# Kernel tuning notes

Hardware: AMD Instinct MI355X
Metric: run time of the kernel (lower is better)

The kernel has to match this reference:

```python
import jax, jax.numpy as jnp
import numpy as np

NUM_BANDS, B, K, D = 5, 512, 64, 200
H = 4            # num attention heads
HID = 512        # selector hidden width
S = 0.02         # weight init scale


def setup_inputs() -> dict:
    key = jax.random.key(0)
    ks = jax.random.split(key, 8)
    F_IN = NUM_BANDS * K * D  # 64000
    return {
        "bands": jax.random.normal(ks[0], (NUM_BANDS, B, K, D), jnp.float32),
        "w1": jax.random.normal(ks[1], (HID, F_IN), jnp.float32) * S,
        "b1": jnp.zeros((HID,), jnp.float32),
        "w2": jax.random.normal(ks[2], (NUM_BANDS, HID), jnp.float32) * S,
        "b2": jnp.zeros((NUM_BANDS,), jnp.float32),
        "in_proj_w": jax.random.normal(ks[3], (3 * D, D), jnp.float32) * S,
        "in_proj_b": jnp.zeros((3 * D,), jnp.float32),
        "out_w": jax.random.normal(ks[4], (D, D), jnp.float32) * S,
        "out_b": jnp.zeros((D,), jnp.float32),
    }


def reference(bands, w1, b1, w2, b2, in_proj_w, in_proj_b, out_w, out_b):
    nb, Bb, k, d = bands.shape
    hd = d // H
    scale = 1.0 / np.sqrt(hd)

    # concat(bands, dim=1): [B, nb*k, d] in band-major order
    x = jnp.transpose(bands, (1, 0, 2, 3))           # [B, nb, k, d]
    kv_in = x.reshape(Bb, nb * k, d)                 # [B, nb*k, d]

    # router MLP + softmax + argmax band select
    flat = kv_in.reshape(Bb, -1)                     # [B, nb*k*d]
    h = jax.nn.relu(flat @ w1.T + b1)                # [B, HID]
    band_weights = jax.nn.softmax(h @ w2.T + b2, axis=-1)
    sel = jnp.argmax(band_weights, axis=-1)          # [B] int

    # gather selected band per sample as the query
    Q = bands[sel, jnp.arange(Bb)]                   # [B, k, d]

    # multihead cross-attention (torch nn.MultiheadAttention math)
    wq, wk, wv = jnp.split(in_proj_w, 3, axis=0)
    bq, bk, bv = jnp.split(in_proj_b, 3, axis=0)
    q = (Q @ wq.T + bq).reshape(Bb, k, H, hd).transpose(0, 2, 1, 3)        # [B,H,k,hd]
    kk = (kv_in @ wk.T + bk).reshape(Bb, nb * k, H, hd).transpose(0, 2, 1, 3)
    v = (kv_in @ wv.T + bv).reshape(Bb, nb * k, H, hd).transpose(0, 2, 1, 3)

    attn = jax.nn.softmax(jnp.einsum('bhqe,bhke->bhqk', q, kk) * scale, axis=-1)
    o = jnp.einsum('bhqk,bhke->bhqe', attn, v)       # [B,H,k,hd]
    o = o.transpose(0, 2, 1, 3).reshape(Bb, k, d)
    return o @ out_w.T + out_b                        # [B, k, d]
```

## Files before the change

### kernel.cpp

```cpp
#include <hip/hip_runtime.h>
#include <hip/hip_bf16.h>

#define NBANDS 5
#define BATCH  512
#define KQN    64
#define DM     200
#define NHEAD  4
#define HD     50
#define HIDW   512
#define TKV    320
#define FIN    64000
#define KSPLIT 20
#define KCH    3200
#define RCH    50
#define NTT    13
#define KST    7
#define NTKV   25

typedef __bf16  bf16x8 __attribute__((ext_vector_type(8)));
typedef float   f32x4  __attribute__((ext_vector_type(4)));

static __device__ inline unsigned short f2bf(float f) {
    __hip_bfloat16 h = __float2bfloat16(f);
    return *reinterpret_cast<unsigned short*>(&h);
}
static __device__ inline float bf2f(unsigned short u) {
    union { unsigned int i; float f; } x;
    x.i = ((unsigned int)u) << 16;
    return x.f;
}
static __device__ inline bf16x8 bf8zero() {
    union { bf16x8 v; unsigned int u[4]; } z;
    z.u[0] = z.u[1] = z.u[2] = z.u[3] = 0u;
    return z.v;
}
static __device__ inline void split8(const float4& a, const float4& b,
                                     bf16x8& hi, bf16x8& lo) {
    union { bf16x8 v; unsigned short u[8]; } H, L;
    const float xs[8] = {a.x, a.y, a.z, a.w, b.x, b.y, b.z, b.w};
#pragma unroll
    for (int i = 0; i < 8; ++i) {
        H.u[i] = f2bf(xs[i]);
        L.u[i] = f2bf(xs[i] - bf2f(H.u[i]));
    }
    hi = H.v; lo = L.v;
}
static __device__ inline bf16x8 round8(const float4& a, const float4& b) {
    union { bf16x8 v; unsigned short u[8]; } H;
    const float xs[8] = {a.x, a.y, a.z, a.w, b.x, b.y, b.z, b.w};
#pragma unroll
    for (int i = 0; i < 8; ++i) H.u[i] = f2bf(xs[i]);
    return H.v;
}

__global__ __launch_bounds__(256) void k_router_mfma(
    const float* __restrict__ bands, const float* __restrict__ w1,
    float* __restrict__ part)
{
    __shared__ __align__(16) unsigned short Ah[64][72];
    __shared__ __align__(16) unsigned short Al[64][72];
    __shared__ __align__(16) unsigned short Bh[64][72];
    __shared__ __align__(16) unsigned short Bl[64][72];

    const int lin     = (blockIdx.z << 6) + (blockIdx.y << 3) + blockIdx.x;
    const int logical = (lin & 7) * 160 + (lin >> 3);
    const int z   = logical >> 6;
    const int rem = logical & 63;
    const int j0  = (rem & 7) << 6;
    const int b0  = (rem >> 3) << 6;

    const int t  = threadIdx.x;
    const int w  = t >> 6, lane = t & 63;
    const int lm = lane & 15, quad = lane >> 4;
    const int m0 = w * 16;

    const int row0 = t >> 4, c4 = (t & 15) * 4;

    f32x4 acc[4];
#pragma unroll
    for (int nt = 0; nt < 4; ++nt) acc[nt] = (f32x4){0.f, 0.f, 0.f, 0.f};

    const int kbase = z * KCH;
    for (int chunk = 0; chunk < RCH; ++chunk) {
        const int kc = kbase + chunk * 64;
        const int band = kc / 12800;
        const float* abase = bands + (size_t)band * 6540800 + kc + c4;
        const float* bbase = w1 + (size_t)j0 * FIN + kc + c4;
        float4 av[4], bv[4];
#pragma unroll
        for (int r = 0; r < 4; ++r)
            av[r] = *(const float4*)(abase + (size_t)(b0 + row0 + r * 16) * 12800);
#pragma unroll
        for (int r = 0; r < 4; ++r)
            bv[r] = *(const float4*)(bbase + (size_t)(row0 + r * 16) * FIN);
        __syncthreads();
#pragma unroll
        for (int r = 0; r < 4; ++r) {
            const int row = row0 + r * 16;
            ushort4 hh, ll;
            hh.x = f2bf(av[r].x); ll.x = f2bf(av[r].x - bf2f(hh.x));
            hh.y = f2bf(av[r].y); ll.y = f2bf(av[r].y - bf2f(hh.y));
            hh.z = f2bf(av[r].z); ll.z = f2bf(av[r].z - bf2f(hh.z));
            hh.w = f2bf(av[r].w); ll.w = f2bf(av[r].w - bf2f(hh.w));
            *(ushort4*)&Ah[row][c4] = hh;
            *(ushort4*)&Al[row][c4] = ll;
        }
#pragma unroll
        for (int r = 0; r < 4; ++r) {
            const int row = row0 + r * 16;
            ushort4 hh, ll;
            hh.x = f2bf(bv[r].x); ll.x = f2bf(bv[r].x - bf2f(hh.x));
            hh.y = f2bf(bv[r].y); ll.y = f2bf(bv[r].y - bf2f(hh.y));
            hh.z = f2bf(bv[r].z); ll.z = f2bf(bv[r].z - bf2f(hh.z));
            hh.w = f2bf(bv[r].w); ll.w = f2bf(bv[r].w - bf2f(hh.w));
            *(ushort4*)&Bh[row][c4] = hh;
            *(ushort4*)&Bl[row][c4] = ll;
        }
        __syncthreads();
#pragma unroll
        for (int ks = 0; ks < 2; ++ks) {
            const int ka = ks * 32 + quad * 8;
            const bf16x8 a_h = *(const bf16x8*)&Ah[m0 + lm][ka];
            const bf16x8 a_l = *(const bf16x8*)&Al[m0 + lm][ka];
#pragma unroll
            for (int nt = 0; nt < 4; ++nt) {
                const bf16x8 b_h = *(const bf16x8*)&Bh[nt * 16 + lm][ka];
                const bf16x8 b_l = *(const bf16x8*)&Bl[nt * 16 + lm][ka];
                acc[nt] = __builtin_amdgcn_mfma_f32_16x16x32_bf16(a_h, b_h, acc[nt], 0, 0, 0);
                acc[nt] = __builtin_amdgcn_mfma_f32_16x16x32_bf16(a_l, b_h, acc[nt], 0, 0, 0);
                acc[nt] = __builtin_amdgcn_mfma_f32_16x16x32_bf16(a_h, b_l, acc[nt], 0, 0, 0);
            }
        }
    }
    float* po = part + (size_t)z * (BATCH * HIDW);
#pragma unroll
    for (int nt = 0; nt < 4; ++nt) {
        const int jj = j0 + nt * 16 + lm;
#pragma unroll
        for (int reg = 0; reg < 4; ++reg) {
            const int bb = b0 + m0 + quad * 4 + reg;
            po[(size_t)bb * HIDW + jj] = acc[nt][reg];
        }
    }
}

__global__ __launch_bounds__(256) void k_reduce_relu(
    const float* __restrict__ part, const float* __restrict__ b1,
    float* __restrict__ h)
{
    const int tid = blockIdx.x * 256 + threadIdx.x;
    float s = b1[tid & (HIDW - 1)];
#pragma unroll
    for (int z = 0; z < KSPLIT; ++z) s += part[z * (BATCH * HIDW) + tid];
    h[tid] = fmaxf(s, 0.f);
}

__global__ __launch_bounds__(256) void k_wpack(
    const float* __restrict__ ipw, const float* __restrict__ outw,
    unsigned short* __restrict__ WqHp, unsigned short* __restrict__ WqLp,
    unsigned short* __restrict__ OwHp, unsigned short* __restrict__ OwLp)
{
    const int p = blockIdx.x;
    const int ks = p / NTT, nt = p - ks * NTT;
    const int t = threadIdx.x;
    const int lane = t >> 2, e0 = (t & 3) * 2;
    const int lm = lane & 15, quad = lane >> 4;
    const int row = nt * 16 + lm;
    const int k  = ks * 32 + quad * 8 + e0;
    const float* src = (blockIdx.y == 0) ? ipw : outw;
    unsigned short* dh = (blockIdx.y == 0) ? WqHp : OwHp;
    unsigned short* dl = (blockIdx.y == 0) ? WqLp : OwLp;
    float v0 = 0.f, v1 = 0.f;
    if (row < DM && k < DM) {
        v0 = src[(size_t)row * DM + k];
        v1 = src[(size_t)row * DM + k + 1];
    }
    const int off = (p << 9) + (lane << 3) + e0;
    const unsigned short h0 = f2bf(v0), h1 = f2bf(v1);
    dh[off]     = h0;
    dh[off + 1] = h1;
    dl[off]     = f2bf(v0 - bf2f(h0));
    dl[off + 1] = f2bf(v1 - bf2f(h1));
}

__global__ __launch_bounds__(256) void k_wpack_kv(
    const float* __restrict__ ipw, unsigned short* __restrict__ Wkv)
{
    const int p = blockIdx.x;
    const int ks = p / NTKV, nt = p - ks * NTKV;
    const int t = threadIdx.x;
    const int lane = t >> 2, e0 = (t & 3) * 2;
    const int lm = lane & 15, quad = lane >> 4;
    const int row = nt * 16 + lm;
    const int k  = ks * 32 + quad * 8 + e0;
    float v0 = 0.f, v1 = 0.f;
    if (k < DM) {
        v0 = ipw[(size_t)(DM + row) * DM + k];
        v1 = ipw[(size_t)(DM + row) * DM + k + 1];
    }
    const int off = (p << 9) + (lane << 3) + e0;
    Wkv[off]     = f2bf(v0);
    Wkv[off + 1] = f2bf(v1);
}

__global__ __launch_bounds__(256) void k_argmax(
    const float* __restrict__ h, const float* __restrict__ w2,
    const float* __restrict__ b2, int* __restrict__ sel)
{
    __shared__ float red[NBANDS][256];
    const int b = blockIdx.x, t = threadIdx.x;
    float acc[NBANDS] = {0.f, 0.f, 0.f, 0.f, 0.f};
    for (int j = t; j < HIDW; j += 256) {
        const float hv = h[b * HIDW + j];
#pragma unroll
        for (int n = 0; n < NBANDS; ++n)
            acc[n] = fmaf(hv, w2[n * HIDW + j], acc[n]);
    }
#pragma unroll
    for (int n = 0; n < NBANDS; ++n) red[n][t] = acc[n];
    __syncthreads();
    for (int s = 128; s > 0; s >>= 1) {
        if (t < s) {
#pragma unroll
            for (int n = 0; n < NBANDS; ++n) red[n][t] += red[n][t + s];
        }
        __syncthreads();
    }
    if (t == 0) {
        int best = 0;
        float bv = red[0][0] + b2[0];
        for (int n = 1; n < NBANDS; ++n) {
            const float v = red[n][0] + b2[n];
            if (v > bv) { bv = v; best = n; }
        }
        sel[b] = best;
    }
}

template<bool BF16OUT>
static __device__ inline void proj_core(
    const float* __restrict__ x0,
    const unsigned short* __restrict__ Ph,
    const unsigned short* __restrict__ Pl,
    const float* __restrict__ bias,
    void* __restrict__ outp)
{
    const int t = threadIdx.x;
    const int w = t >> 6, lane = t & 63;
    const int lm = lane & 15, quad = lane >> 4;
    const int m0 = w * 16;
    const float* xrow = x0 + (size_t)(m0 + lm) * DM;

    f32x4 acc[NTT];
#pragma unroll
    for (int nt = 0; nt < NTT; ++nt) acc[nt] = (f32x4){0.f, 0.f, 0.f, 0.f};

#pragma unroll
    for (int ks = 0; ks < KST; ++ks) {
        const int k0 = ks * 32 + quad * 8;
        bf16x8 a_h = bf8zero(), a_l = bf8zero();
        if (k0 + 8 <= DM) {
            const float4 xa = *(const float4*)(xrow + k0);
            const float4 xb = *(const float4*)(xrow + k0 + 4);
            split8(xa, xb, a_h, a_l);
        }
        const unsigned short* ph = Ph + ((ks * NTT) << 9) + (lane << 3);
        const unsigned short* pl = Pl + ((ks * NTT) << 9) + (lane << 3);
#pragma unroll
        for (int nt = 0; nt < NTT; ++nt) {
            const bf16x8 b_h = *(const bf16x8*)(ph + (nt << 9));
            const bf16x8 b_l = *(const bf16x8*)(pl + (nt << 9));
            acc[nt] = __builtin_amdgcn_mfma_f32_16x16x32_bf16(a_h, b_h, acc[nt], 0, 0, 0);
            acc[nt] = __builtin_amdgcn_mfma_f32_16x16x32_bf16(a_l, b_h, acc[nt], 0, 0, 0);
            acc[nt] = __builtin_amdgcn_mfma_f32_16x16x32_bf16(a_h, b_l, acc[nt], 0, 0, 0);
        }
    }
#pragma unroll
    for (int nt = 0; nt < NTT; ++nt) {
        const int col = nt * 16 + lm;
        if (col < DM) {
            const float bs = bias[col];
#pragma unroll
            for (int reg = 0; reg < 4; ++reg) {
                const int row = m0 + quad * 4 + reg;
                const float v = acc[nt][reg] + bs;
                if (BF16OUT)
                    ((unsigned short*)outp)[(size_t)row * DM + col] = f2bf(v);
                else
                    ((float*)outp)[(size_t)row * DM + col] = v;
            }
        }
    }
}

__global__ __launch_bounds__(256) void k_qproj_mfma(
    const float* __restrict__ bands, const int* __restrict__ sel,
    const unsigned short* __restrict__ WqHp, const unsigned short* __restrict__ WqLp,
    const float* __restrict__ ipb, unsigned short* __restrict__ qb)
{
    const int b = blockIdx.x;
    const int band = sel[b];
    const float* x0 = bands + (size_t)((band * BATCH + b) * KQN) * DM;
    proj_core<true>(x0, WqHp, WqLp, ipb, qb + (size_t)(b * KQN) * DM);
}

__global__ __launch_bounds__(256) void k_outproj_mfma(
    const float* __restrict__ obuf, const unsigned short* __restrict__ OwHp,
    const unsigned short* __restrict__ OwLp, const float* __restrict__ outb,
    float* __restrict__ out)
{
    const int b = blockIdx.x;
    proj_core<false>(obuf + (size_t)(b * KQN) * DM, OwHp, OwLp, outb,
                     out + (size_t)(b * KQN) * DM);
}

__global__ __launch_bounds__(256) void k_kvproj_lds(
    const float* __restrict__ bands, const unsigned short* __restrict__ Wkv,
    const float* __restrict__ ipb, __hip_bfloat16* __restrict__ Kp,
    __hip_bfloat16* __restrict__ Vp)
{
    __shared__ __align__(16) unsigned short Bs[2][NTKV * 512];
    const int t = threadIdx.x;
    const int w = t >> 6, lane = t & 63;
    const int lm = lane & 15, quad = lane >> 4;
    const int m0 = w * 16;
    const int M0 = blockIdx.x * 64;

    const int gg = M0 + m0 + lm;
    const int bb = gg / TKV, tk = gg - bb * TKV;
    const int band = tk >> 6, kk = tk & 63;
    const float* xrow = bands + (size_t)((band * BATCH + bb) * KQN + kk) * DM;

    float4 ar[2 * KST];
#pragma unroll
    for (int ks = 0; ks < KST; ++ks) {
        const int k0 = ks * 32 + quad * 8;
        if (k0 + 8 <= DM) {
            ar[2 * ks]     = *(const float4*)(xrow + k0);
            ar[2 * ks + 1] = *(const float4*)(xrow + k0 + 4);
        }
    }
    bf16x8 a[KST];
#pragma unroll
    for (int ks = 0; ks < KST; ++ks) {
        const int k0 = ks * 32 + quad * 8;
        a[ks] = (k0 + 8 <= DM) ? round8(ar[2 * ks], ar[2 * ks + 1]) : bf8zero();
    }

    auto stage = [&](int ks, int buf) {
        const unsigned short* src = Wkv + ((ks * NTKV) << 9);
#pragma unroll
        for (int pass = 0; pass < 6; ++pass) {
            const int i = pass * 256 + t;
            __builtin_amdgcn_global_load_lds(
                (const __attribute__((address_space(1))) unsigned int*)(src + (size_t)i * 8),
                (__attribute__((address_space(3))) unsigned int*)&Bs[buf][(pass * 256 + w * 64) * 8],
                16, 0, 0);
        }
        if (t < 64) {
            __builtin_amdgcn_global_load_lds(
                (const __attribute__((address_space(1))) unsigned int*)(src + (size_t)(1536 + lane) * 8),
                (__attribute__((address_space(3))) unsigned int*)&Bs[buf][1536 * 8],
                16, 0, 0);
        }
    };

    f32x4 acc[NTKV];
#pragma unroll
    for (int nt = 0; nt < NTKV; ++nt) acc[nt] = (f32x4){0.f, 0.f, 0.f, 0.f};

    stage(0, 0);
    __syncthreads();
#pragma unroll
    for (int ks = 0; ks < KST; ++ks) {
        if (ks + 1 < KST) stage(ks + 1, (ks + 1) & 1);
        const unsigned short* bs = &Bs[ks & 1][lane * 8];
#pragma unroll
        for (int nt = 0; nt < NTKV; ++nt) {
            const bf16x8 b8 = *(const bf16x8*)(bs + (nt << 9));
            acc[nt] = __builtin_amdgcn_mfma_f32_16x16x32_bf16(a[ks], b8, acc[nt], 0, 0, 0);
        }
        __syncthreads();
    }

#pragma unroll
    for (int nt = 0; nt < NTKV; ++nt) {
        const int col = nt * 16 + lm;
        const float bias = ipb[DM + col];
#pragma unroll
        for (int reg = 0; reg < 4; ++reg) {
            const int grow = M0 + m0 + quad * 4 + reg;
            const float v = acc[nt][reg] + bias;
            if (col < DM) Kp[(size_t)grow * DM + col] = __float2bfloat16(v);
            else          Vp[(size_t)grow * DM + (col - DM)] = __float2bfloat16(v);
        }
    }
}

__global__ __launch_bounds__(256) void k_attn(
    const unsigned short* __restrict__ qb, const __hip_bfloat16* __restrict__ Kp,
    const __hip_bfloat16* __restrict__ Vp, float* __restrict__ obuf)
{
    __shared__ __align__(16) unsigned short Qs[64][72];
    __shared__ __align__(16) unsigned short KP[320][72];
    __shared__ __align__(16) unsigned short Vt[64][328];
    __shared__ __align__(16) unsigned short Ps[64][328];
    const int b = blockIdx.x, hh = blockIdx.y;
    const int t = threadIdx.x;

    const unsigned short* qbase = qb + (size_t)(b * KQN) * DM + hh * HD;
    for (int idx = t; idx < 64 * 64; idx += 256) {
        const int r = idx >> 6, e = idx & 63;
        Qs[r][e] = (e < HD) ? qbase[(size_t)r * DM + e] : 0;
    }
    const unsigned short* kbase = (const unsigned short*)Kp + (size_t)b * TKV * DM + hh * HD;
    for (int idx = t; idx < 320 * 25; idx += 256) {
        const int key = idx / 25, g = idx - key * 25;
        *(unsigned int*)&KP[key][g * 2] =
            *(const unsigned int*)(kbase + (size_t)key * DM + g * 2);
    }
    for (int idx = t; idx < 320 * 7; idx += 256) {
        const int key = idx / 7, g = idx - key * 7;
        *(unsigned int*)&KP[key][50 + g * 2] = 0;
    }
    const unsigned short* vbase = (const unsigned short*)Vp + (size_t)b * TKV * DM + hh * HD;
    for (int idx = t; idx < 320 * 25; idx += 256) {
        const int key = idx / 25, g = idx - key * 25;
        const unsigned int v = *(const unsigned int*)(vbase + (size_t)key * DM + g * 2);
        Vt[g * 2][key]     = (unsigned short)(v & 0xffffu);
        Vt[g * 2 + 1][key] = (unsigned short)(v >> 16);
    }
    __syncthreads();

    const int w = t >> 6, lane = t & 63;
    const int lm = lane & 15, quad = lane >> 4;
    const int m0 = w * 16;

    f32x4 s[20];
#pragma unroll
    for (int nt = 0; nt < 20; ++nt) s[nt] = (f32x4){0.f, 0.f, 0.f, 0.f};
#pragma unroll
    for (int ks = 0; ks < 2; ++ks) {
        const int ka = ks * 32 + quad * 8;
        const bf16x8 a = *(const bf16x8*)&Qs[m0 + lm][ka];
#pragma unroll
        for (int nt = 0; nt < 20; ++nt) {
            const bf16x8 bb8 = *(const bf16x8*)&KP[nt * 16 + lm][ka];
            s[nt] = __builtin_amdgcn_mfma_f32_16x16x32_bf16(a, bb8, s[nt], 0, 0, 0);
        }
    }

    const float scale = 0.14142135623730951f;
    float inv[4];
#pragma unroll
    for (int reg = 0; reg < 4; ++reg) {
        float mx = -1e30f;
#pragma unroll
        for (int nt = 0; nt < 20; ++nt) {
            const float sv = s[nt][reg] * scale;
            s[nt][reg] = sv;
            mx = fmaxf(mx, sv);
        }
#pragma unroll
        for (int off = 1; off < 16; off <<= 1)
            mx = fmaxf(mx, __shfl_xor(mx, off, 64));
        float lsum = 0.f;
#pragma unroll
        for (int nt = 0; nt < 20; ++nt) {
            const float p = __expf(s[nt][reg] - mx);
            s[nt][reg] = p;
            lsum += p;
        }
#pragma unroll
        for (int off = 1; off < 16; off <<= 1)
            lsum += __shfl_xor(lsum, off, 64);
        inv[reg] = 1.f / lsum;
    }
#pragma unroll
    for (int reg = 0; reg < 4; ++reg) {
        const int row = m0 + quad * 4 + reg;
#pragma unroll
        for (int nt = 0; nt < 20; ++nt)
            Ps[row][nt * 16 + lm] = f2bf(s[nt][reg]);
    }
    __syncthreads();

    f32x4 o[4];
#pragma unroll
    for (int nt = 0; nt < 4; ++nt) o[nt] = (f32x4){0.f, 0.f, 0.f, 0.f};
#pragma unroll
    for (int ks = 0; ks < 10; ++ks) {
        const int ka = ks * 32 + quad * 8;
        const bf16x8 a = *(const bf16x8*)&Ps[m0 + lm][ka];
#pragma unroll
        for (int nt = 0; nt < 4; ++nt) {
            const bf16x8 bb8 = *(const bf16x8*)&Vt[nt * 16 + lm][ka];
            o[nt] = __builtin_amdgcn_mfma_f32_16x16x32_bf16(a, bb8, o[nt], 0, 0, 0);
        }
    }
    float* op = obuf + (size_t)(b * KQN) * DM + hh * HD;
#pragma unroll
    for (int nt = 0; nt < 4; ++nt) {
        const int e = nt * 16 + lm;
        if (e < HD) {
#pragma unroll
            for (int reg = 0; reg < 4; ++reg) {
                const int row = m0 + quad * 4 + reg;
                op[(size_t)row * DM + e] = o[nt][reg] * inv[reg];
            }
        }
    }
}

extern "C" void kernel_launch(void* const* d_in, const int* in_sizes, int n_in,
                              void* d_out, int out_size, void* d_ws, size_t ws_size,
                              hipStream_t stream)
{
    const float* bands = (const float*)d_in[0];
    const float* w1    = (const float*)d_in[1];
    const float* b1    = (const float*)d_in[2];
    const float* w2    = (const float*)d_in[3];
    const float* b2    = (const float*)d_in[4];
    const float* ipw   = (const float*)d_in[5];
    const float* ipb   = (const float*)d_in[6];
    const float* outw  = (const float*)d_in[7];
    const float* outb  = (const float*)d_in[8];
    float* out = (float*)d_out;

    if (ws_size < (size_t)192940032) return;

    char* ws = (char*)d_ws;
    int*   sel  = (int*)  (ws + 0);
    float* part = (float*)(ws + 4096);
    float* h    = (float*)(ws + 20975616);
    unsigned short* qb = (unsigned short*)(ws + 4096);
    unsigned short* Wkv  = (unsigned short*)(ws + 26218496);
    unsigned short* WqHp = (unsigned short*)(ws + 26404096);
    unsigned short* WqLp = (unsigned short*)(ws + 26497280);
    unsigned short* OwHp = (unsigned short*)(ws + 26590464);
    unsigned short* OwLp = (unsigned short*)(ws + 26683648);
    __hip_bfloat16* Kp = (__hip_bfloat16*)(ws + 26776832);
    __hip_bfloat16* Vp = (__hip_bfloat16*)(ws + 92312832);
    float* obuf = (float*)(ws + 157848832);

    k_wpack_kv<<<KST * NTKV, 256, 0, stream>>>(ipw, Wkv);
    k_wpack<<<dim3(KST * NTT, 2), 256, 0, stream>>>(ipw, outw, WqHp, WqLp, OwHp, OwLp);

    k_router_mfma<<<dim3(8, 8, KSPLIT), 256, 0, stream>>>(bands, w1, part);
    k_reduce_relu<<<(BATCH * HIDW) / 256, 256, 0, stream>>>(part, b1, h);
    k_argmax<<<BATCH, 256, 0, stream>>>(h, w2, b2, sel);
    k_qproj_mfma<<<BATCH, 256, 0, stream>>>(bands, sel, WqHp, WqLp, ipb, qb);
    k_kvproj_lds<<<2560, 256, 0, stream>>>(bands, Wkv, ipb, Kp, Vp);
    k_attn<<<dim3(BATCH, NHEAD), 256, 0, stream>>>(qb, Kp, Vp, obuf);
    k_outproj_mfma<<<BATCH, 256, 0, stream>>>(obuf, OwHp, OwLp, outb, out);
}
```

Before: 782.8 us.

## Pre-split w1 into MFMA-packed bf16 hi/lo tiles and drop LDS from router GEMM

Adds a kernel that converts w1 once per call into hi/lo bf16 halves stored in MFMA fragment order. The router GEMM then reads B fragments straight from global memory and splits A in registers, with no LDS staging or barriers. It also widens the tile to 64x128, doubles the K-split to 40, and sets launch bounds to 3 blocks per SM. The intent is to avoid converting w1 repeatedly across batch tiles and to remove sync overhead, at the cost of an extra 128MB of packed-weight traffic, more partial sums to reduce, and global loads that are no longer shared through LDS.

```diff
diff --git a/kernel.cpp b/kernel.cpp
--- a/kernel.cpp
+++ b/kernel.cpp
@@ -10,9 +10,10 @@
 #define HIDW   512
 #define TKV    320
 #define FIN    64000
-#define KSPLIT 20
-#define KCH    3200
-#define RCH    50
+#define BSTRIDE 6553600
+#define KSPLIT 40
+#define KCH    1600
+#define RCH    25
 #define NTT    13
 #define KST    7
 #define NTKV   25
@@ -53,88 +54,101 @@
     return H.v;
 }
 
-__global__ __launch_bounds__(256) void k_router_mfma(
-    const float* __restrict__ bands, const float* __restrict__ w1,
-    float* __restrict__ part)
-{
-    __shared__ __align__(16) unsigned short Ah[64][72];
-    __shared__ __align__(16) unsigned short Al[64][72];
-    __shared__ __align__(16) unsigned short Bh[64][72];
-    __shared__ __align__(16) unsigned short Bl[64][72];
-
-    const int lin     = (blockIdx.z << 6) + (blockIdx.y << 3) + blockIdx.x;
+__global__ __launch_bounds__(256) void k_splitw1(
+    const float* __restrict__ w1, unsigned short* __restrict__ BHp,
+    unsigned short* __restrict__ BLp)
+{
+    __shared__ __align__(16) unsigned short Hs[128][72];
+    __shared__ __align__(16) unsigned short Ls[128][72];
+    const int kc = blockIdx.x;
+    const int jt = blockIdx.y;
+    const int t  = threadIdx.x;
+    const int rl0 = t >> 4, cl4 = (t & 15) * 4;
+#pragma unroll
+    for (int i = 0; i < 8; ++i) {
+        const int row = rl0 + i * 16;
+        const float4 v = *(const float4*)(w1
+            + (size_t)(jt * 128 + row) * FIN + kc * 64 + cl4);
+        ushort4 hh, ll;
+        hh.x = f2bf(v.x); ll.x = f2bf(v.x - bf2f(hh.x));
+        hh.y = f2bf(v.y); ll.y = f2bf(v.y - bf2f(hh.y));
+        hh.z = f2bf(v.z); ll.z = f2bf(v.z - bf2f(hh.z));
+        hh.w = f2bf(v.w); ll.w = f2bf(v.w - bf2f(hh.w));
+        *(ushort4*)&Hs[row][cl4] = hh;
+        *(ushort4*)&Ls[row][cl4] = ll;
+    }
+    __syncthreads();
+    const size_t tbase = ((size_t)(jt * 1000 + kc)) << 13;
+#pragma unroll
+    for (int i = 0; i < 4; ++i) {
+        const int slot = i * 256 + t;
+        const int ksnt = slot >> 6, lane = slot & 63;
+        const int ks = ksnt >> 3, nt = ksnt & 7;
+        const int row = nt * 16 + (lane & 15);
+        const int col = ks * 32 + (lane >> 4) * 8;
+        *(uint4*)(BHp + tbase + (size_t)slot * 8) = *(const uint4*)&Hs[row][col];
+        *(uint4*)(BLp + tbase + (size_t)slot * 8) = *(const uint4*)&Ls[row][col];
+    }
+}
+
+__global__ __launch_bounds__(256, 3) void k_router_mfma(
+    const float* __restrict__ bands, const unsigned short* __restrict__ BHp,
+    const unsigned short* __restrict__ BLp, float* __restrict__ part)
+{
+    const int lin = (blockIdx.z << 5) | (blockIdx.y << 2) | blockIdx.x;
     const int logical = (lin & 7) * 160 + (lin >> 3);
-    const int z   = logical >> 6;
-    const int rem = logical & 63;
-    const int j0  = (rem & 7) << 6;
-    const int b0  = (rem >> 3) << 6;
-
-    const int t  = threadIdx.x;
-    const int w  = t >> 6, lane = t & 63;
+    const int z   = logical >> 5;
+    const int rem = logical & 31;
+    const int bt  = rem >> 2, jt = rem & 3;
+    const int b0  = bt << 6, j0 = jt << 7;
+
+    const int t = threadIdx.x;
+    const int w = t >> 6, lane = t & 63;
     const int lm = lane & 15, quad = lane >> 4;
-    const int m0 = w * 16;
-
-    const int row0 = t >> 4, c4 = (t & 15) * 4;
-
-    f32x4 acc[4];
-#pragma unroll
-    for (int nt = 0; nt < 4; ++nt) acc[nt] = (f32x4){0.f, 0.f, 0.f, 0.f};
-
-    const int kbase = z * KCH;
+    const int m0 = w << 4;
+
+    const float* xrow = bands + (size_t)(z >> 3) * BSTRIDE
+                      + (size_t)(b0 + m0 + lm) * 12800 + (z & 7) * KCH
+                      + quad * 8;
+    const size_t tile0 = ((size_t)(jt * 1000 + z * RCH)) << 13;
+    const unsigned short* hb = BHp + tile0 + lane * 8;
+    const unsigned short* lb = BLp + tile0 + lane * 8;
+
+    f32x4 acc[8];
+#pragma unroll
+    for (int nt = 0; nt < 8; ++nt) acc[nt] = (f32x4){0.f, 0.f, 0.f, 0.f};
+
     for (int chunk = 0; chunk < RCH; ++chunk) {
-        const int kc = kbase + chunk * 64;
-        const int band = kc / 12800;
-        const float* abase = bands + (size_t)band * 6540800 + kc + c4;
-        const float* bbase = w1 + (size_t)j0 * FIN + kc + c4;
-        float4 av[4], bv[4];
-#pragma unroll
-        for (int r = 0; r < 4; ++r)
-            av[r] = *(const float4*)(abase + (size_t)(b0 + row0 + r * 16) * 12800);
-#pragma unroll
-        for (int r = 0; r < 4; ++r)
-            bv[r] = *(const float4*)(bbase + (size_t)(row0 + r * 16) * FIN);
-        __syncthreads();
-#pragma unroll
-        for (int r = 0; r < 4; ++r) {
-            const int row = row0 + r * 16;
-            ushort4 hh, ll;
-            hh.x = f2bf(av[r].x); ll.x = f2bf(av[r].x - bf2f(hh.x));
-            hh.y = f2bf(av[r].y); ll.y = f2bf(av[r].y - bf2f(hh.y));
-            hh.z = f2bf(av[r].z); ll.z = f2bf(av[r].z - bf2f(hh.z));
-            hh.w = f2bf(av[r].w); ll.w = f2bf(av[r].w - bf2f(hh.w));
-            *(ushort4*)&Ah[row][c4] = hh;
-            *(ushort4*)&Al[row][c4] = ll;
-        }
-#pragma unroll
-        for (int r = 0; r < 4; ++r) {
-            const int row = row0 + r * 16;
-            ushort4 hh, ll;
-            hh.x = f2bf(bv[r].x); ll.x = f2bf(bv[r].x - bf2f(hh.x));
-            hh.y = f2bf(bv[r].y); ll.y = f2bf(bv[r].y - bf2f(hh.y));
-            hh.z = f2bf(bv[r].z); ll.z = f2bf(bv[r].z - bf2f(hh.z));
-            hh.w = f2bf(bv[r].w); ll.w = f2bf(bv[r].w - bf2f(hh.w));
-            *(ushort4*)&Bh[row][c4] = hh;
-            *(ushort4*)&Bl[row][c4] = ll;
-        }
-        __syncthreads();
-#pragma unroll
-        for (int ks = 0; ks < 2; ++ks) {
-            const int ka = ks * 32 + quad * 8;
-            const bf16x8 a_h = *(const bf16x8*)&Ah[m0 + lm][ka];
-            const bf16x8 a_l = *(const bf16x8*)&Al[m0 + lm][ka];
-#pragma unroll
-            for (int nt = 0; nt < 4; ++nt) {
-                const bf16x8 b_h = *(const bf16x8*)&Bh[nt * 16 + lm][ka];
-                const bf16x8 b_l = *(const bf16x8*)&Bl[nt * 16 + lm][ka];
-                acc[nt] = __builtin_amdgcn_mfma_f32_16x16x32_bf16(a_h, b_h, acc[nt], 0, 0, 0);
-                acc[nt] = __builtin_amdgcn_mfma_f32_16x16x32_bf16(a_l, b_h, acc[nt], 0, 0, 0);
-                acc[nt] = __builtin_amdgcn_mfma_f32_16x16x32_bf16(a_h, b_l, acc[nt], 0, 0, 0);
-            }
+        const float* ap = xrow + chunk * 64;
+        const float4 a00 = *(const float4*)(ap);
+        const float4 a01 = *(const float4*)(ap + 4);
+        const float4 a10 = *(const float4*)(ap + 32);
+        const float4 a11 = *(const float4*)(ap + 36);
+        bf16x8 ah0, al0, ah1, al1;
+        split8(a00, a01, ah0, al0);
+        split8(a10, a11, ah1, al1);
+        const unsigned short* hc = hb + ((size_t)chunk << 13);
+        const unsigned short* lc = lb + ((size_t)chunk << 13);
+#pragma unroll
+        for (int nt = 0; nt < 8; ++nt) {
+            const bf16x8 bh = *(const bf16x8*)(hc + (nt << 9));
+            const bf16x8 bl = *(const bf16x8*)(lc + (nt << 9));
+            acc[nt] = __builtin_amdgcn_mfma_f32_16x16x32_bf16(ah0, bh, acc[nt], 0, 0, 0);
+            acc[nt] = __builtin_amdgcn_mfma_f32_16x16x32_bf16(al0, bh, acc[nt], 0, 0, 0);
+            acc[nt] = __builtin_amdgcn_mfma_f32_16x16x32_bf16(ah0, bl, acc[nt], 0, 0, 0);
+        }
+#pragma unroll
+        for (int nt = 0; nt < 8; ++nt) {
+            const bf16x8 bh = *(const bf16x8*)(hc + ((8 + nt) << 9));
+            const bf16x8 bl = *(const bf16x8*)(lc + ((8 + nt) << 9));
+            acc[nt] = __builtin_amdgcn_mfma_f32_16x16x32_bf16(ah1, bh, acc[nt], 0, 0, 0);
+            acc[nt] = __builtin_amdgcn_mfma_f32_16x16x32_bf16(al1, bh, acc[nt], 0, 0, 0);
+            acc[nt] = __builtin_amdgcn_mfma_f32_16x16x32_bf16(ah1, bl, acc[nt], 0, 0, 0);
         }
     }
     float* po = part + (size_t)z * (BATCH * HIDW);
 #pragma unroll
-    for (int nt = 0; nt < 4; ++nt) {
+    for (int nt = 0; nt < 8; ++nt) {
         const int jj = j0 + nt * 16 + lm;
 #pragma unroll
         for (int reg = 0; reg < 4; ++reg) {
@@ -150,7 +164,7 @@
 {
     const int tid = blockIdx.x * 256 + threadIdx.x;
     float s = b1[tid & (HIDW - 1)];
-#pragma unroll
+#pragma unroll 8
     for (int z = 0; z < KSPLIT; ++z) s += part[z * (BATCH * HIDW) + tid];
     h[tid] = fmaxf(s, 0.f);
 }
@@ -531,22 +545,25 @@
 
     char* ws = (char*)d_ws;
     int*   sel  = (int*)  (ws + 0);
-    float* part = (float*)(ws + 4096);
-    float* h    = (float*)(ws + 20975616);
-    unsigned short* qb = (unsigned short*)(ws + 4096);
-    unsigned short* Wkv  = (unsigned short*)(ws + 26218496);
-    unsigned short* WqHp = (unsigned short*)(ws + 26404096);
-    unsigned short* WqLp = (unsigned short*)(ws + 26497280);
-    unsigned short* OwHp = (unsigned short*)(ws + 26590464);
-    unsigned short* OwLp = (unsigned short*)(ws + 26683648);
-    __hip_bfloat16* Kp = (__hip_bfloat16*)(ws + 26776832);
-    __hip_bfloat16* Vp = (__hip_bfloat16*)(ws + 92312832);
+    unsigned short* BHp  = (unsigned short*)(ws + 4096);
+    unsigned short* BLp  = (unsigned short*)(ws + 65540096);
+    float* part = (float*)(ws + 131076096);
+    float* h    = (float*)(ws + 173019136);
+    unsigned short* qb   = (unsigned short*)(ws + 4096);
+    __hip_bfloat16* Kp   = (__hip_bfloat16*)(ws + 26776832);
+    __hip_bfloat16* Vp   = (__hip_bfloat16*)(ws + 92312832);
     float* obuf = (float*)(ws + 157848832);
+    unsigned short* Wkv  = (unsigned short*)(ws + 184063232);
+    unsigned short* WqHp = (unsigned short*)(ws + 184242432);
+    unsigned short* WqLp = (unsigned short*)(ws + 184335616);
+    unsigned short* OwHp = (unsigned short*)(ws + 184428800);
+    unsigned short* OwLp = (unsigned short*)(ws + 184521984);
 
     k_wpack_kv<<<KST * NTKV, 256, 0, stream>>>(ipw, Wkv);
     k_wpack<<<dim3(KST * NTT, 2), 256, 0, stream>>>(ipw, outw, WqHp, WqLp, OwHp, OwLp);
-
-    k_router_mfma<<<dim3(8, 8, KSPLIT), 256, 0, stream>>>(bands, w1, part);
+    k_splitw1<<<dim3(1000, 4), 256, 0, stream>>>(w1, BHp, BLp);
+
+    k_router_mfma<<<dim3(4, 8, KSPLIT), 256, 0, stream>>>(bands, BHp, BLp, part);
     k_reduce_relu<<<(BATCH * HIDW) / 256, 256, 0, stream>>>(part, b1, h);
     k_argmax<<<BATCH, 256, 0, stream>>>(h, w2, b2, sel);
     k_qproj_mfma<<<BATCH, 256, 0, stream>>>(bands, sel, WqHp, WqLp, ipb, qb);
```

Result: slower. 892.8 us (+14.1%).
